# Kernel tuning notes

Measured on AMD Instinct MI355X. Metric: run time of the kernel, lower is better.

The kernel has to match this reference:

```python
import jax, jax.numpy as jnp
import numpy as np

INPUT_DIM, HIDDEN, NUM_CLASSES = 16, 128, 24
B, T = 4096, 1024  # raw I/Q frame (B, 2, T); seq_len = 2*T/INPUT_DIM = 128


def setup_inputs() -> dict:
    key = jax.random.key(0)
    ks = jax.random.split(key, 12)
    s = 1.0 / np.sqrt(HIDDEN)  # torch default uniform bound ~ use scaled normal
    def w(k, shape, scale):
        return jax.random.normal(k, shape, jnp.float32) * scale
    return {
        "x": jax.random.normal(ks[0], (B, 2, T), jnp.float32),
        "w_ih1": w(ks[1], (3 * HIDDEN, INPUT_DIM), s),
        "w_hh1": w(ks[2], (3 * HIDDEN, HIDDEN), s),
        "b_ih1": w(ks[3], (3 * HIDDEN,), s),
        "b_hh1": w(ks[4], (3 * HIDDEN,), s),
        "w_ih2": w(ks[5], (3 * HIDDEN, HIDDEN), s),
        "w_hh2": w(ks[6], (3 * HIDDEN, HIDDEN), s),
        "b_ih2": w(ks[7], (3 * HIDDEN,), s),
        "b_hh2": w(ks[8], (3 * HIDDEN,), s),
        "fc_w": w(ks[9], (NUM_CLASSES, HIDDEN), s),
        "fc_b": w(ks[10], (NUM_CLASSES,), s),
    }


def _gru_layer(x, w_ih, w_hh, b_ih, b_hh, return_seq=True):
    # x: (B, L, D). PyTorch GRU gate order: r, z, n.
    Bb = x.shape[0]
    H = w_hh.shape[1]
    xp = jnp.einsum('bld,gd->blg', x, w_ih) + b_ih  # (B, L, 3H) precomputed input proj

    def step(h, xt):
        gh = h @ w_hh.T + b_hh  # (B, 3H)
        ir, iz, inn = jnp.split(xt, 3, axis=-1)
        hr, hz, hn = jnp.split(gh, 3, axis=-1)
        r = jax.nn.sigmoid(ir + hr)
        z = jax.nn.sigmoid(iz + hz)
        n = jnp.tanh(inn + r * hn)
        h_new = (1.0 - z) * n + z * h
        return h_new, (h_new if return_seq else 0.0)

    h0 = jnp.zeros((Bb, H), x.dtype)
    h_last, ys = jax.lax.scan(step, h0, jnp.swapaxes(xp, 0, 1))
    if return_seq:
        return jnp.swapaxes(ys, 0, 1)
    return h_last


def reference(x, w_ih1, w_hh1, b_ih1, b_hh1, w_ih2, w_hh2, b_ih2, b_hh2, fc_w, fc_b):
    Bb = x.shape[0]
    # (B,2,T) -> (B,2,L,8) -> (B,L,2,8) -> (B,L,16)
    h = x.reshape(Bb, 2, -1, INPUT_DIM // 2)
    h = jnp.swapaxes(h, 1, 2).reshape(Bb, -1, INPUT_DIM)
    seq1 = _gru_layer(h, w_ih1, w_hh1, b_ih1, b_hh1, return_seq=True)
    last = _gru_layer(seq1, w_ih2, w_hh2, b_ih2, b_hh2, return_seq=False)
    return last @ fc_w.T + fc_b
```

## Files before the change

### kernel.cpp

```cpp
#include <hip/hip_runtime.h>


typedef _Float16 half_t;
typedef _Float16 half8 __attribute__((ext_vector_type(8)));
typedef _Float16 half4v __attribute__((ext_vector_type(4)));
typedef float f32x4 __attribute__((ext_vector_type(4)));

#define BB 16
#define HS 136
#define XS 520

static __device__ __forceinline__ f32x4 mfma16(half8 a, half8 b, f32x4 c) {
  return __builtin_amdgcn_mfma_f32_16x16x32_f16(a, b, c, 0, 0, 0);
}

static __device__ __forceinline__ half8 zero8() {
  half8 v;
#pragma unroll
  for (int i = 0; i < 8; ++i) v[i] = (half_t)0.f;
  return v;
}

static __device__ __forceinline__ half8 ldw8(const float* __restrict__ p) {
  float4 a = *(const float4*)p;
  float4 b = *(const float4*)(p + 4);
  half8 r;
  r[0] = (half_t)a.x; r[1] = (half_t)a.y; r[2] = (half_t)a.z; r[3] = (half_t)a.w;
  r[4] = (half_t)b.x; r[5] = (half_t)b.y; r[6] = (half_t)b.z; r[7] = (half_t)b.w;
  return r;
}

static __device__ __forceinline__ float sigm(float v) {
  return __builtin_amdgcn_rcpf(1.f + __expf(-v));
}
static __device__ __forceinline__ float tanh_fast(float v) {
  float e = __expf(2.f * v);
  return 1.f - 2.f * __builtin_amdgcn_rcpf(1.f + e);
}

__global__ __launch_bounds__(512, 2) void gru_l1(
    const float* __restrict__ x,
    const float* __restrict__ wih1, const float* __restrict__ whh1,
    const float* __restrict__ bih1, const float* __restrict__ bhh1,
    half_t* __restrict__ seq1)
{
  __shared__ __align__(16) half_t xl[BB][XS];
  __shared__ __align__(16) half_t ost[8][BB][HS];

  const int tid = threadIdx.x;
  const int lane = tid & 63;
  const int wv = tid >> 6;
  const int q = lane >> 4;
  const int c = lane & 15;
  const int jc = wv * 16 + c;
  const int s0 = blockIdx.x * BB;

  for (int i = tid; i < 8 * BB * HS; i += 512) ((half_t*)ost)[i] = (half_t)0.f;

  const float b1r  = bih1[jc]       + bhh1[jc];
  const float b1z  = bih1[128 + jc] + bhh1[128 + jc];
  const float b1in = bih1[256 + jc];
  const float b1hn = bhh1[256 + jc];

  half8 wi1r, wi1z, wi1n;
  if (q < 2) {
    wi1r = ldw8(wih1 + (0 * 128 + jc) * 16 + q * 8);
    wi1z = ldw8(wih1 + (1 * 128 + jc) * 16 + q * 8);
    wi1n = ldw8(wih1 + (2 * 128 + jc) * 16 + q * 8);
  } else {
    wi1r = zero8(); wi1z = zero8(); wi1n = zero8();
  }
  half8 wh1r[4], wh1z[4], wh1n[4];
#pragma unroll
  for (int kk = 0; kk < 4; ++kk) {
    const int ko = kk * 32 + q * 8;
    wh1r[kk] = ldw8(whh1 + (0 * 128 + jc) * 128 + ko);
    wh1z[kk] = ldw8(whh1 + (1 * 128 + jc) * 128 + ko);
    wh1n[kk] = ldw8(whh1 + (2 * 128 + jc) * 128 + ko);
  }

  float h1p[4] = {0.f, 0.f, 0.f, 0.f};

  for (int g = 0; g < 16; ++g) {
    if ((g & 3) == 0) {
      const int tc = g >> 2;
#pragma unroll
      for (int it = 0; it < 4; ++it) {
        int idx = tid + it * 512;
        int s = idx >> 7;
        int rem = idx & 127;
        int ch = rem >> 6;
        int i4 = rem & 63;
        const float4 v = *(const float4*)(x + (size_t)(s0 + s) * 2048 + ch * 1024 + tc * 256 + i4 * 4);
        half4v hv;
        hv[0] = (half_t)v.x; hv[1] = (half_t)v.y; hv[2] = (half_t)v.z; hv[3] = (half_t)v.w;
        *(half4v*)&xl[s][(i4 >> 1) * 16 + ch * 8 + (i4 & 1) * 4] = hv;
      }
      __syncthreads();
    }

    for (int tt = 0; tt < 8; ++tt) {
      const int i = g * 8 + tt;
      const int prev = (i + 7) & 7;

      f32x4 ar  = {b1r, b1r, b1r, b1r};
      f32x4 az  = {b1z, b1z, b1z, b1z};
      f32x4 ain = {b1in, b1in, b1in, b1in};
      f32x4 ahn = {b1hn, b1hn, b1hn, b1hn};
      {
        half8 ax = zero8();
        if (q < 2) ax = *(const half8*)&xl[c][(i & 31) * 16 + q * 8];
        ar  = mfma16(ax, wi1r, ar);
        az  = mfma16(ax, wi1z, az);
        ain = mfma16(ax, wi1n, ain);
      }
#pragma unroll
      for (int kk = 0; kk < 4; ++kk) {
        half8 ah = *(const half8*)&ost[prev][c][kk * 32 + q * 8];
        ar  = mfma16(ah, wh1r[kk], ar);
        az  = mfma16(ah, wh1z[kk], az);
        ahn = mfma16(ah, wh1n[kk], ahn);
      }
#pragma unroll
      for (int r = 0; r < 4; ++r) {
        float rg = sigm(ar[r]);
        float zg = sigm(az[r]);
        float ng = tanh_fast(fmaf(rg, ahn[r], ain[r]));
        float hn = fmaf(zg, h1p[r] - ng, ng);
        h1p[r] = hn;
        ost[tt][q * 4 + r][jc] = (half_t)hn;
      }
      __syncthreads();
    }

#pragma unroll
    for (int p = 0; p < 4; ++p) {
      int idx = tid + p * 512;
      int col16 = idx & 15;
      int row = (idx >> 4) & 15;
      int st = idx >> 8;
      f32x4 v = *(const f32x4*)&ost[st][row][col16 * 8];
      size_t off = ((size_t)((s0 + row) * 128 + (g * 8 + st))) * 128 + col16 * 8;
      *(f32x4*)(seq1 + off) = v;
    }
    __syncthreads();
  }
}

__global__ __launch_bounds__(512, 2) void gru_l2(
    const half_t* __restrict__ seq1,
    const float* __restrict__ wih2, const float* __restrict__ whh2,
    const float* __restrict__ bih2, const float* __restrict__ bhh2,
    const float* __restrict__ fcw, const float* __restrict__ fcb,
    float* __restrict__ out)
{
  __shared__ __align__(16) half_t sc[2][8][BB][HS];
  __shared__ __align__(16) half_t h2b[2][BB][HS];
  __shared__ float h2f[BB][129];

  const int tid = threadIdx.x;
  const int lane = tid & 63;
  const int wv = tid >> 6;
  const int q = lane >> 4;
  const int c = lane & 15;
  const int jc = wv * 16 + c;
  const int s0 = blockIdx.x * BB;

  for (int i = tid; i < BB * HS; i += 512) ((half_t*)h2b[0])[i] = (half_t)0.f;

  const float b2r  = bih2[jc]       + bhh2[jc];
  const float b2z  = bih2[128 + jc] + bhh2[128 + jc];
  const float b2in = bih2[256 + jc];
  const float b2hn = bhh2[256 + jc];

  half8 wi2r[4], wi2z[4], wi2n[4], wh2r[4], wh2z[4], wh2n[4];
#pragma unroll
  for (int kk = 0; kk < 4; ++kk) {
    const int ko = kk * 32 + q * 8;
    wi2r[kk] = ldw8(wih2 + (0 * 128 + jc) * 128 + ko);
    wi2z[kk] = ldw8(wih2 + (1 * 128 + jc) * 128 + ko);
    wi2n[kk] = ldw8(wih2 + (2 * 128 + jc) * 128 + ko);
    wh2r[kk] = ldw8(whh2 + (0 * 128 + jc) * 128 + ko);
    wh2z[kk] = ldw8(whh2 + (1 * 128 + jc) * 128 + ko);
    wh2n[kk] = ldw8(whh2 + (2 * 128 + jc) * 128 + ko);
  }

#pragma unroll
  for (int p = 0; p < 4; ++p) {
    int idx = tid + p * 512;
    int col16 = idx & 15;
    int row = (idx >> 4) & 15;
    int st = idx >> 8;
    size_t off = ((size_t)((s0 + row) * 128 + st)) * 128 + col16 * 8;
    *(f32x4*)&sc[0][st][row][col16 * 8] = *(const f32x4*)(seq1 + off);
  }
  __syncthreads();

  float h2p[4] = {0.f, 0.f, 0.f, 0.f};

  for (int ch = 0; ch < 16; ++ch) {
    f32x4 pf[4];
    if (ch < 15) {
#pragma unroll
      for (int p = 0; p < 4; ++p) {
        int idx = tid + p * 512;
        int col16 = idx & 15;
        int row = (idx >> 4) & 15;
        int st = idx >> 8;
        size_t off = ((size_t)((s0 + row) * 128 + ((ch + 1) * 8 + st))) * 128 + col16 * 8;
        pf[p] = *(const f32x4*)(seq1 + off);
      }
    }
    const int cb = ch & 1;

    for (int tt = 0; tt < 8; ++tt) {
      const int i = ch * 8 + tt;
      const int rb = i & 1;
      const int wb = rb ^ 1;

      f32x4 cr  = {b2r, b2r, b2r, b2r};
      f32x4 cz  = {b2z, b2z, b2z, b2z};
      f32x4 cin = {b2in, b2in, b2in, b2in};
      f32x4 chn = {b2hn, b2hn, b2hn, b2hn};
#pragma unroll
      for (int kk = 0; kk < 4; ++kk) {
        half8 a1 = *(const half8*)&sc[cb][tt][c][kk * 32 + q * 8];
        half8 a2 = *(const half8*)&h2b[rb][c][kk * 32 + q * 8];
        cr  = mfma16(a1, wi2r[kk], cr);
        cz  = mfma16(a1, wi2z[kk], cz);
        cin = mfma16(a1, wi2n[kk], cin);
        cr  = mfma16(a2, wh2r[kk], cr);
        cz  = mfma16(a2, wh2z[kk], cz);
        chn = mfma16(a2, wh2n[kk], chn);
      }
#pragma unroll
      for (int r = 0; r < 4; ++r) {
        float rg = sigm(cr[r]);
        float zg = sigm(cz[r]);
        float ng = tanh_fast(fmaf(rg, chn[r], cin[r]));
        float hn = fmaf(zg, h2p[r] - ng, ng);
        h2p[r] = hn;
        h2b[wb][q * 4 + r][jc] = (half_t)hn;
      }
      if (tt == 7 && ch < 15) {
#pragma unroll
        for (int p = 0; p < 4; ++p) {
          int idx = tid + p * 512;
          int col16 = idx & 15;
          int row = (idx >> 4) & 15;
          int st = idx >> 8;
          *(f32x4*)&sc[cb ^ 1][st][row][col16 * 8] = pf[p];
        }
      }
      __syncthreads();
    }
  }

#pragma unroll
  for (int r = 0; r < 4; ++r) h2f[q * 4 + r][jc] = h2p[r];
  __syncthreads();
  if (tid < 384) {
    const int m = tid & 15;
    const int cls = tid >> 4;
    const float* w = fcw + cls * 128;
    float acc = fcb[cls];
#pragma unroll 8
    for (int j = 0; j < 128; ++j) acc = fmaf(h2f[m][j], w[j], acc);
    out[(size_t)(s0 + m) * 24 + cls] = acc;
  }
}

__global__ __launch_bounds__(512, 2) void gru_fused(
    const float* __restrict__ x,
    const float* __restrict__ wih1, const float* __restrict__ whh1,
    const float* __restrict__ bih1, const float* __restrict__ bhh1,
    const float* __restrict__ wih2, const float* __restrict__ whh2,
    const float* __restrict__ bih2, const float* __restrict__ bhh2,
    const float* __restrict__ fcw, const float* __restrict__ fcb,
    float* __restrict__ out)
{
  __shared__ __align__(16) half_t xl[BB][XS];
  __shared__ __align__(16) half_t h1b[2][BB][HS];
  __shared__ __align__(16) half_t h2b[2][BB][HS];
  __shared__ float h2f[BB][129];

  const int tid = threadIdx.x;
  const int lane = tid & 63;
  const int wv = tid >> 6;
  const int q = lane >> 4;
  const int c = lane & 15;
  const int jc = wv * 16 + c;
  const int s0 = blockIdx.x * BB;

  for (int i = tid; i < 2 * BB * HS; i += 512) {
    ((half_t*)h1b)[i] = (half_t)0.f;
    ((half_t*)h2b)[i] = (half_t)0.f;
  }

  const float b1r  = bih1[jc]       + bhh1[jc];
  const float b1z  = bih1[128 + jc] + bhh1[128 + jc];
  const float b1in = bih1[256 + jc];
  const float b1hn = bhh1[256 + jc];
  const float b2r  = bih2[jc]       + bhh2[jc];
  const float b2z  = bih2[128 + jc] + bhh2[128 + jc];
  const float b2in = bih2[256 + jc];
  const float b2hn = bhh2[256 + jc];

  half8 wi1r, wi1z, wi1n;
  if (q < 2) {
    wi1r = ldw8(wih1 + (0 * 128 + jc) * 16 + q * 8);
    wi1z = ldw8(wih1 + (1 * 128 + jc) * 16 + q * 8);
    wi1n = ldw8(wih1 + (2 * 128 + jc) * 16 + q * 8);
  } else {
    wi1r = zero8(); wi1z = zero8(); wi1n = zero8();
  }
  half8 wh1r[4], wh1z[4], wh1n[4], wi2r[4], wi2z[4], wi2n[4], wh2r[4], wh2z[4], wh2n[4];
#pragma unroll
  for (int kk = 0; kk < 4; ++kk) {
    const int ko = kk * 32 + q * 8;
    wh1r[kk] = ldw8(whh1 + (0 * 128 + jc) * 128 + ko);
    wh1z[kk] = ldw8(whh1 + (1 * 128 + jc) * 128 + ko);
    wh1n[kk] = ldw8(whh1 + (2 * 128 + jc) * 128 + ko);
    wi2r[kk] = ldw8(wih2 + (0 * 128 + jc) * 128 + ko);
    wi2z[kk] = ldw8(wih2 + (1 * 128 + jc) * 128 + ko);
    wi2n[kk] = ldw8(wih2 + (2 * 128 + jc) * 128 + ko);
    wh2r[kk] = ldw8(whh2 + (0 * 128 + jc) * 128 + ko);
    wh2z[kk] = ldw8(whh2 + (1 * 128 + jc) * 128 + ko);
    wh2n[kk] = ldw8(whh2 + (2 * 128 + jc) * 128 + ko);
  }

  float h1p[4] = {0.f, 0.f, 0.f, 0.f};
  float h2p[4] = {0.f, 0.f, 0.f, 0.f};

  for (int tc = 0; tc < 4; ++tc) {
#pragma unroll
    for (int it = 0; it < 4; ++it) {
      int idx = tid + it * 512;
      int s = idx >> 7;
      int rem = idx & 127;
      int ch = rem >> 6;
      int i4 = rem & 63;
      const float4 v = *(const float4*)(x + (size_t)(s0 + s) * 2048 + ch * 1024 + tc * 256 + i4 * 4);
      half4v hv;
      hv[0] = (half_t)v.x; hv[1] = (half_t)v.y; hv[2] = (half_t)v.z; hv[3] = (half_t)v.w;
      *(half4v*)&xl[s][(i4 >> 1) * 16 + ch * 8 + (i4 & 1) * 4] = hv;
    }
    __syncthreads();

    for (int tt = 0; tt < 32; ++tt) {
      const int i = tc * 32 + tt;
      const int rb = i & 1;
      const int wb = rb ^ 1;

      f32x4 ar  = {b1r, b1r, b1r, b1r};
      f32x4 az  = {b1z, b1z, b1z, b1z};
      f32x4 ain = {b1in, b1in, b1in, b1in};
      f32x4 ahn = {b1hn, b1hn, b1hn, b1hn};
      f32x4 cr  = {b2r, b2r, b2r, b2r};
      f32x4 cz  = {b2z, b2z, b2z, b2z};
      f32x4 cin = {b2in, b2in, b2in, b2in};
      f32x4 chn = {b2hn, b2hn, b2hn, b2hn};

      {
        half8 ax = zero8();
        if (q < 2) ax = *(const half8*)&xl[c][tt * 16 + q * 8];
        ar  = mfma16(ax, wi1r, ar);
        az  = mfma16(ax, wi1z, az);
        ain = mfma16(ax, wi1n, ain);
      }
#pragma unroll
      for (int kk = 0; kk < 4; ++kk) {
        half8 ah = *(const half8*)&h1b[rb][c][kk * 32 + q * 8];
        half8 a2 = *(const half8*)&h2b[rb][c][kk * 32 + q * 8];
        ar  = mfma16(ah, wh1r[kk], ar);
        az  = mfma16(ah, wh1z[kk], az);
        ahn = mfma16(ah, wh1n[kk], ahn);
        cr  = mfma16(ah, wi2r[kk], cr);
        cz  = mfma16(ah, wi2z[kk], cz);
        cin = mfma16(ah, wi2n[kk], cin);
        cr  = mfma16(a2, wh2r[kk], cr);
        cz  = mfma16(a2, wh2z[kk], cz);
        chn = mfma16(a2, wh2n[kk], chn);
      }

#pragma unroll
      for (int r = 0; r < 4; ++r) {
        float rg = sigm(ar[r]);
        float zg = sigm(az[r]);
        float ng = tanh_fast(fmaf(rg, ahn[r], ain[r]));
        float hn = fmaf(zg, h1p[r] - ng, ng);
        h1p[r] = hn;
        h1b[wb][q * 4 + r][jc] = (half_t)hn;
      }
      if (i > 0) {
#pragma unroll
        for (int r = 0; r < 4; ++r) {
          float rg = sigm(cr[r]);
          float zg = sigm(cz[r]);
          float ng = tanh_fast(fmaf(rg, chn[r], cin[r]));
          float hn = fmaf(zg, h2p[r] - ng, ng);
          h2p[r] = hn;
          h2b[wb][q * 4 + r][jc] = (half_t)hn;
        }
      }
      __syncthreads();
    }
  }

  {
    f32x4 cr  = {b2r, b2r, b2r, b2r};
    f32x4 cz  = {b2z, b2z, b2z, b2z};
    f32x4 cin = {b2in, b2in, b2in, b2in};
    f32x4 chn = {b2hn, b2hn, b2hn, b2hn};
#pragma unroll
    for (int kk = 0; kk < 4; ++kk) {
      half8 a1 = *(const half8*)&h1b[0][c][kk * 32 + q * 8];
      half8 a2 = *(const half8*)&h2b[0][c][kk * 32 + q * 8];
      cr  = mfma16(a1, wi2r[kk], cr);
      cz  = mfma16(a1, wi2z[kk], cz);
      cin = mfma16(a1, wi2n[kk], cin);
      cr  = mfma16(a2, wh2r[kk], cr);
      cz  = mfma16(a2, wh2z[kk], cz);
      chn = mfma16(a2, wh2n[kk], chn);
    }
#pragma unroll
    for (int r = 0; r < 4; ++r) {
      float rg = sigm(cr[r]);
      float zg = sigm(cz[r]);
      float ng = tanh_fast(fmaf(rg, chn[r], cin[r]));
      h2p[r] = fmaf(zg, h2p[r] - ng, ng);
    }
  }

#pragma unroll
  for (int r = 0; r < 4; ++r) h2f[q * 4 + r][jc] = h2p[r];
  __syncthreads();
  if (tid < 384) {
    const int m = tid & 15;
    const int cls = tid >> 4;
    const float* w = fcw + cls * 128;
    float acc = fcb[cls];
#pragma unroll 8
    for (int j = 0; j < 128; ++j) acc = fmaf(h2f[m][j], w[j], acc);
    out[(size_t)(s0 + m) * 24 + cls] = acc;
  }
}

extern "C" void kernel_launch(void* const* d_in, const int* in_sizes, int n_in,
                              void* d_out, int out_size, void* d_ws, size_t ws_size,
                              hipStream_t stream) {
  (void)in_sizes; (void)n_in; (void)out_size;
  const float* x    = (const float*)d_in[0];
  const float* wih1 = (const float*)d_in[1];
  const float* whh1 = (const float*)d_in[2];
  const float* bih1 = (const float*)d_in[3];
  const float* bhh1 = (const float*)d_in[4];
  const float* wih2 = (const float*)d_in[5];
  const float* whh2 = (const float*)d_in[6];
  const float* bih2 = (const float*)d_in[7];
  const float* bhh2 = (const float*)d_in[8];
  const float* fcw  = (const float*)d_in[9];
  const float* fcb  = (const float*)d_in[10];
  float* outp = (float*)d_out;

  const size_t seq_bytes = (size_t)4096 * 128 * 128 * sizeof(half_t);
  if (ws_size >= seq_bytes) {
    half_t* seq1 = (half_t*)d_ws;
    gru_l1<<<dim3(256), dim3(512), 0, stream>>>(x, wih1, whh1, bih1, bhh1, seq1);
    gru_l2<<<dim3(256), dim3(512), 0, stream>>>(seq1, wih2, whh2, bih2, bhh2, fcw, fcb, outp);
  } else {
    gru_fused<<<dim3(256), dim3(512), 0, stream>>>(
        x, wih1, whh1, bih1, bhh1, wih2, whh2, bih2, bhh2, fcw, fcb, outp);
  }
}
```

Measured before the change: 295.9 us.

## Halve per-block batch to 8 sequences and double grid for two blocks per CU

Each block of the layer-1 and layer-2 GRU kernels now processes 8 sequences instead of 16, with the unused MFMA rows zero-padded, and the grid doubles to 512 blocks. Launch bounds request four waves per SIMD so two blocks can share a CU and overlap their serial recurrence latency. The layer-2 prefetch chunk shrinks to 4 timesteps and the tt loops are unrolled. The trade is half-wasted MFMA throughput and tighter register limits that risk spilling the register-resident weights.

```diff
diff --git a/kernel.cpp b/kernel.cpp
--- a/kernel.cpp
+++ b/kernel.cpp
@@ -6,7 +6,6 @@
 typedef _Float16 half4v __attribute__((ext_vector_type(4)));
 typedef float f32x4 __attribute__((ext_vector_type(4)));
 
-#define BB 16
 #define HS 136
 #define XS 520
 
@@ -38,14 +37,14 @@
   return 1.f - 2.f * __builtin_amdgcn_rcpf(1.f + e);
 }
 
-__global__ __launch_bounds__(512, 2) void gru_l1(
+__global__ __launch_bounds__(512, 4) void gru_l1(
     const float* __restrict__ x,
     const float* __restrict__ wih1, const float* __restrict__ whh1,
     const float* __restrict__ bih1, const float* __restrict__ bhh1,
     half_t* __restrict__ seq1)
 {
-  __shared__ __align__(16) half_t xl[BB][XS];
-  __shared__ __align__(16) half_t ost[8][BB][HS];
+  __shared__ __align__(16) half_t xl[16][XS];
+  __shared__ __align__(16) half_t ost[8][16][HS];
 
   const int tid = threadIdx.x;
   const int lane = tid & 63;
@@ -53,9 +52,10 @@
   const int q = lane >> 4;
   const int c = lane & 15;
   const int jc = wv * 16 + c;
-  const int s0 = blockIdx.x * BB;
-
-  for (int i = tid; i < 8 * BB * HS; i += 512) ((half_t*)ost)[i] = (half_t)0.f;
+  const int s0 = blockIdx.x * 8;
+
+  for (int i = tid; i < 8 * 16 * HS; i += 512) ((half_t*)ost)[i] = (half_t)0.f;
+  for (int i = tid; i < 8 * XS; i += 512) xl[8 + (i / XS)][i % XS] = (half_t)0.f;
 
   const float b1r  = bih1[jc]       + bhh1[jc];
   const float b1z  = bih1[128 + jc] + bhh1[128 + jc];
@@ -80,12 +80,13 @@
   }
 
   float h1p[4] = {0.f, 0.f, 0.f, 0.f};
+  __syncthreads();
 
   for (int g = 0; g < 16; ++g) {
     if ((g & 3) == 0) {
       const int tc = g >> 2;
 #pragma unroll
-      for (int it = 0; it < 4; ++it) {
+      for (int it = 0; it < 2; ++it) {
         int idx = tid + it * 512;
         int s = idx >> 7;
         int rem = idx & 127;
@@ -99,9 +100,10 @@
       __syncthreads();
     }
 
+#pragma unroll
     for (int tt = 0; tt < 8; ++tt) {
-      const int i = g * 8 + tt;
-      const int prev = (i + 7) & 7;
+      const int t = g * 8 + tt;
+      const int prev = (tt + 7) & 7;
 
       f32x4 ar  = {b1r, b1r, b1r, b1r};
       f32x4 az  = {b1z, b1z, b1z, b1z};
@@ -109,7 +111,7 @@
       f32x4 ahn = {b1hn, b1hn, b1hn, b1hn};
       {
         half8 ax = zero8();
-        if (q < 2) ax = *(const half8*)&xl[c][(i & 31) * 16 + q * 8];
+        if (q < 2) ax = *(const half8*)&xl[c][(t & 31) * 16 + q * 8];
         ar  = mfma16(ax, wi1r, ar);
         az  = mfma16(ax, wi1z, az);
         ain = mfma16(ax, wi1n, ain);
@@ -134,11 +136,11 @@
     }
 
 #pragma unroll
-    for (int p = 0; p < 4; ++p) {
+    for (int p = 0; p < 2; ++p) {
       int idx = tid + p * 512;
       int col16 = idx & 15;
-      int row = (idx >> 4) & 15;
-      int st = idx >> 8;
+      int row = (idx >> 4) & 7;
+      int st = idx >> 7;
       f32x4 v = *(const f32x4*)&ost[st][row][col16 * 8];
       size_t off = ((size_t)((s0 + row) * 128 + (g * 8 + st))) * 128 + col16 * 8;
       *(f32x4*)(seq1 + off) = v;
@@ -147,16 +149,16 @@
   }
 }
 
-__global__ __launch_bounds__(512, 2) void gru_l2(
+__global__ __launch_bounds__(512, 4) void gru_l2(
     const half_t* __restrict__ seq1,
     const float* __restrict__ wih2, const float* __restrict__ whh2,
     const float* __restrict__ bih2, const float* __restrict__ bhh2,
     const float* __restrict__ fcw, const float* __restrict__ fcb,
     float* __restrict__ out)
 {
-  __shared__ __align__(16) half_t sc[2][8][BB][HS];
-  __shared__ __align__(16) half_t h2b[2][BB][HS];
-  __shared__ float h2f[BB][129];
+  __shared__ __align__(16) half_t sc[2][4][16][HS];
+  __shared__ __align__(16) half_t h2b[2][16][HS];
+  __shared__ float h2f[8][132];
 
   const int tid = threadIdx.x;
   const int lane = tid & 63;
@@ -164,9 +166,10 @@
   const int q = lane >> 4;
   const int c = lane & 15;
   const int jc = wv * 16 + c;
-  const int s0 = blockIdx.x * BB;
-
-  for (int i = tid; i < BB * HS; i += 512) ((half_t*)h2b[0])[i] = (half_t)0.f;
+  const int s0 = blockIdx.x * 8;
+
+  for (int i = tid; i < 2 * 4 * 16 * HS; i += 512) ((half_t*)sc)[i] = (half_t)0.f;
+  for (int i = tid; i < 2 * 16 * HS; i += 512) ((half_t*)h2b)[i] = (half_t)0.f;
 
   const float b2r  = bih2[jc]       + bhh2[jc];
   const float b2z  = bih2[128 + jc] + bhh2[128 + jc];
@@ -184,38 +187,33 @@
     wh2z[kk] = ldw8(whh2 + (1 * 128 + jc) * 128 + ko);
     wh2n[kk] = ldw8(whh2 + (2 * 128 + jc) * 128 + ko);
   }
-
-#pragma unroll
-  for (int p = 0; p < 4; ++p) {
-    int idx = tid + p * 512;
-    int col16 = idx & 15;
-    int row = (idx >> 4) & 15;
-    int st = idx >> 8;
+  __syncthreads();
+
+  {
+    const int col16 = tid & 15;
+    const int row = (tid >> 4) & 7;
+    const int st = tid >> 7;
     size_t off = ((size_t)((s0 + row) * 128 + st)) * 128 + col16 * 8;
     *(f32x4*)&sc[0][st][row][col16 * 8] = *(const f32x4*)(seq1 + off);
   }
   __syncthreads();
 
   float h2p[4] = {0.f, 0.f, 0.f, 0.f};
-
-  for (int ch = 0; ch < 16; ++ch) {
-    f32x4 pf[4];
-    if (ch < 15) {
-#pragma unroll
-      for (int p = 0; p < 4; ++p) {
-        int idx = tid + p * 512;
-        int col16 = idx & 15;
-        int row = (idx >> 4) & 15;
-        int st = idx >> 8;
-        size_t off = ((size_t)((s0 + row) * 128 + ((ch + 1) * 8 + st))) * 128 + col16 * 8;
-        pf[p] = *(const f32x4*)(seq1 + off);
-      }
+  const int col16 = tid & 15;
+  const int prow = (tid >> 4) & 7;
+  const int pst = tid >> 7;
+
+  for (int ch = 0; ch < 32; ++ch) {
+    f32x4 pf;
+    if (ch < 31) {
+      size_t off = ((size_t)((s0 + prow) * 128 + ((ch + 1) * 4 + pst))) * 128 + col16 * 8;
+      pf = *(const f32x4*)(seq1 + off);
     }
     const int cb = ch & 1;
 
-    for (int tt = 0; tt < 8; ++tt) {
-      const int i = ch * 8 + tt;
-      const int rb = i & 1;
+#pragma unroll
+    for (int tt = 0; tt < 4; ++tt) {
+      const int rb = tt & 1;
       const int wb = rb ^ 1;
 
       f32x4 cr  = {b2r, b2r, b2r, b2r};
@@ -242,26 +240,21 @@
         h2p[r] = hn;
         h2b[wb][q * 4 + r][jc] = (half_t)hn;
       }
-      if (tt == 7 && ch < 15) {
-#pragma unroll
-        for (int p = 0; p < 4; ++p) {
-          int idx = tid + p * 512;
-          int col16 = idx & 15;
-          int row = (idx >> 4) & 15;
-          int st = idx >> 8;
-          *(f32x4*)&sc[cb ^ 1][st][row][col16 * 8] = pf[p];
-        }
+      if (tt == 3 && ch < 31) {
+        *(f32x4*)&sc[cb ^ 1][pst][prow][col16 * 8] = pf;
       }
       __syncthreads();
     }
   }
 
-#pragma unroll
-  for (int r = 0; r < 4; ++r) h2f[q * 4 + r][jc] = h2p[r];
+  if (q < 2) {
+#pragma unroll
+    for (int r = 0; r < 4; ++r) h2f[q * 4 + r][jc] = h2p[r];
+  }
   __syncthreads();
-  if (tid < 384) {
-    const int m = tid & 15;
-    const int cls = tid >> 4;
+  if (tid < 192) {
+    const int m = tid & 7;
+    const int cls = tid >> 3;
     const float* w = fcw + cls * 128;
     float acc = fcb[cls];
 #pragma unroll 8
@@ -279,10 +272,10 @@
     const float* __restrict__ fcw, const float* __restrict__ fcb,
     float* __restrict__ out)
 {
-  __shared__ __align__(16) half_t xl[BB][XS];
-  __shared__ __align__(16) half_t h1b[2][BB][HS];
-  __shared__ __align__(16) half_t h2b[2][BB][HS];
-  __shared__ float h2f[BB][129];
+  __shared__ __align__(16) half_t xl[16][XS];
+  __shared__ __align__(16) half_t h1b[2][16][HS];
+  __shared__ __align__(16) half_t h2b[2][16][HS];
+  __shared__ float h2f[16][129];
 
   const int tid = threadIdx.x;
   const int lane = tid & 63;
@@ -290,9 +283,9 @@
   const int q = lane >> 4;
   const int c = lane & 15;
   const int jc = wv * 16 + c;
-  const int s0 = blockIdx.x * BB;
-
-  for (int i = tid; i < 2 * BB * HS; i += 512) {
+  const int s0 = blockIdx.x * 16;
+
+  for (int i = tid; i < 2 * 16 * HS; i += 512) {
     ((half_t*)h1b)[i] = (half_t)0.f;
     ((half_t*)h2b)[i] = (half_t)0.f;
   }
@@ -466,8 +459,8 @@
   const size_t seq_bytes = (size_t)4096 * 128 * 128 * sizeof(half_t);
   if (ws_size >= seq_bytes) {
     half_t* seq1 = (half_t*)d_ws;
-    gru_l1<<<dim3(256), dim3(512), 0, stream>>>(x, wih1, whh1, bih1, bhh1, seq1);
-    gru_l2<<<dim3(256), dim3(512), 0, stream>>>(seq1, wih2, whh2, bih2, bhh2, fcw, fcb, outp);
+    gru_l1<<<dim3(512), dim3(512), 0, stream>>>(x, wih1, whh1, bih1, bhh1, seq1);
+    gru_l2<<<dim3(512), dim3(512), 0, stream>>>(seq1, wih2, whh2, bih2, bhh2, fcw, fcb, outp);
   } else {
     gru_fused<<<dim3(256), dim3(512), 0, stream>>>(
         x, wih1, whh1, bih1, bhh1, wih2, whh2, bih2, bhh2, fcw, fcb, outp);
```

Result: slower. 1.117 ms (+277.5%).
